# Kernel tuning notes

Hardware: AMD Instinct MI355X
Metric: run time of the kernel (lower is better)

The kernel has to match this reference:

```python
import jax, jax.numpy as jnp
import numpy as np

B, S, D, H, F = 2, 2048, 1024, 16, 4096
DH = D // H
EPS = 1e-6


def setup_inputs() -> dict:
    key = jax.random.key(0)
    ks = jax.random.split(key, 8)
    x = jax.random.normal(ks[0], (B, S, D), dtype=jnp.float32)
    # causal mask, broadcastable over [B,H,S,S]
    attention_mask = jnp.tril(jnp.ones((S, S), dtype=bool))[None, None]
    Wqkv = jax.random.normal(ks[1], (3 * D, D), dtype=jnp.float32) * (1.0 / np.sqrt(D))
    Wout = jax.random.normal(ks[2], (D, D), dtype=jnp.float32) * (1.0 / np.sqrt(D))
    W1 = jax.random.normal(ks[3], (F, D), dtype=jnp.float32) * (1.0 / np.sqrt(D))
    b1 = jnp.zeros((F,), dtype=jnp.float32)
    W2 = jax.random.normal(ks[4], (D, F), dtype=jnp.float32) * (1.0 / np.sqrt(F))
    b2 = jnp.zeros((D,), dtype=jnp.float32)
    gamma1 = jnp.ones((D,), dtype=jnp.float32)
    beta1 = jnp.zeros((D,), dtype=jnp.float32)
    gamma2 = jnp.ones((D,), dtype=jnp.float32)
    beta2 = jnp.zeros((D,), dtype=jnp.float32)
    return {"x": x, "attention_mask": attention_mask, "Wqkv": Wqkv, "Wout": Wout,
            "W1": W1, "b1": b1, "W2": W2, "b2": b2,
            "gamma1": gamma1, "beta1": beta1, "gamma2": gamma2, "beta2": beta2}


def layer_norm(x, gamma, beta):
    # Matches torch module: (x - mean) / (std + eps), std unbiased=False
    mean = jnp.mean(x, axis=-1, keepdims=True)
    std = jnp.sqrt(jnp.mean((x - mean) ** 2, axis=-1, keepdims=True))
    return gamma * ((x - mean) / (std + EPS)) + beta


def reference(x, attention_mask, Wqkv, Wout, W1, b1, W2, b2, gamma1, beta1, gamma2, beta2):
    # --- attention sub-block (Pre-LN) ---
    h = layer_norm(x, gamma1, beta1)
    qkv = h @ Wqkv.T                                   # [B,S,3D]
    qkv = qkv.reshape(B, S, 3, H, DH).transpose(2, 0, 3, 1, 4)  # [3,B,H,S,DH]
    q, k, v = qkv[0], qkv[1], qkv[2]
    scale = DH ** -0.5
    scores = jnp.einsum('bhqd,bhkd->bhqk', q, k) * scale
    scores = jnp.where(attention_mask, scores, -jnp.inf)
    attn = jax.nn.softmax(scores, axis=-1)
    out = jnp.einsum('bhqk,bhkd->bhqd', attn, v)       # [B,H,S,DH]
    out = out.transpose(0, 2, 1, 3).reshape(B, S, D)
    out = out @ Wout.T
    x = x + out                                        # dropout eval = identity
    # --- FFN sub-block (Pre-LN) ---
    h = layer_norm(x, gamma2, beta2)
    h = jax.nn.gelu(h @ W1.T + b1, approximate=False)  # torch GELU default = exact erf
    h = h @ W2.T + b2
    return x + h
```

## Files before the change

### kernel.cpp

```cpp
#include <hip/hip_runtime.h>
#include <hip/hip_bf16.h>
#include <math.h>


typedef __bf16 bf16;
typedef __bf16 bf16x4 __attribute__((ext_vector_type(4)));
typedef __bf16 bf16x8 __attribute__((ext_vector_type(8)));
typedef float f32x4 __attribute__((ext_vector_type(4)));

#define LOG2E 1.4426950408889634f
#define NSHIFT -17.312340489f

__device__ __forceinline__ f32x4 mfma16(bf16x8 a, bf16x8 b, f32x4 c) {
    return __builtin_amdgcn_mfma_f32_16x16x32_bf16(a, b, c, 0, 0, 0);
}
__device__ __forceinline__ void load16_lds(const bf16* g, bf16* l) {
    __builtin_amdgcn_global_load_lds(
        (__attribute__((address_space(1))) void*)g,
        (__attribute__((address_space(3))) void*)l, 16, 0, 0);
}

__global__ __launch_bounds__(256) void cvt4_kernel(const float* __restrict__ s0,
                                                   const float* __restrict__ s1,
                                                   const float* __restrict__ s2,
                                                   const float* __restrict__ s3,
                                                   bf16* __restrict__ dst) {
    const int blk = blockIdx.x;
    const float* s;
    int base;
    if (blk < 3072)      { s = s0; base = blk * 1024; }
    else if (blk < 4096) { s = s1; base = (blk - 3072) * 1024; }
    else if (blk < 8192) { s = s2; base = (blk - 4096) * 1024; }
    else                 { s = s3; base = (blk - 8192) * 1024; }
    const int t4 = threadIdx.x * 4;
    const float4 f = *(const float4*)(s + base + t4);
    bf16x4 o;
    o[0] = (bf16)f.x; o[1] = (bf16)f.y; o[2] = (bf16)f.z; o[3] = (bf16)f.w;
    *(bf16x4*)(dst + (size_t)blk * 1024 + t4) = o;
}

__global__ __launch_bounds__(256) void ln_kernel(const float* __restrict__ xin,
                                                 bf16* __restrict__ out,
                                                 const float* __restrict__ gamma,
                                                 const float* __restrict__ beta) {
    const int row = blockIdx.x;
    const int tid = threadIdx.x;
    const float4 f = *(const float4*)(xin + (size_t)row * 1024 + tid * 4);
    float v[4] = {f.x, f.y, f.z, f.w};
    float s = v[0] + v[1] + v[2] + v[3];
    float s2 = v[0] * v[0] + v[1] * v[1] + v[2] * v[2] + v[3] * v[3];
#pragma unroll
    for (int off = 1; off < 64; off <<= 1) {
        s += __shfl_xor(s, off);
        s2 += __shfl_xor(s2, off);
    }
    __shared__ float red[8];
    const int wave = tid >> 6, lane = tid & 63;
    if (lane == 0) { red[wave] = s; red[4 + wave] = s2; }
    __syncthreads();
    s = red[0] + red[1] + red[2] + red[3];
    s2 = red[4] + red[5] + red[6] + red[7];
    const float mean = s * (1.0f / 1024.0f);
    float var = s2 * (1.0f / 1024.0f) - mean * mean;
    var = fmaxf(var, 0.0f);
    const float rstd = 1.0f / (sqrtf(var) + 1e-6f);
    const int c = tid * 4;
    const float4 g = *(const float4*)(gamma + c);
    const float4 b = *(const float4*)(beta + c);
    bf16x4 o;
    o[0] = (bf16)((v[0] - mean) * rstd * g.x + b.x);
    o[1] = (bf16)((v[1] - mean) * rstd * g.y + b.y);
    o[2] = (bf16)((v[2] - mean) * rstd * g.z + b.z);
    o[3] = (bf16)((v[3] - mean) * rstd * g.w + b.w);
    *(bf16x4*)(out + (size_t)row * 1024 + c) = o;
}

#define STAGE(tt, bi)                                              \
    do {                                                           \
        const int _k0 = (tt) << 5;                                 \
        load16_lds(Ap + _k0, &As[bi][tid * 8]);                    \
        load16_lds(Bp + _k0, &Bs[bi][tid * 8]);                    \
        load16_lds(Ap + rstep + _k0, &As[bi][tid * 8 + 2048]);     \
        load16_lds(Bp + rstep + _k0, &Bs[bi][tid * 8 + 2048]);     \
    } while (0)

__global__ __launch_bounds__(256, 3) void gemm_res(const bf16* __restrict__ A,
                                                   const bf16* __restrict__ B,
                                                   int N, int K, int ldk,
                                                   float* __restrict__ outf,
                                                   const float* __restrict__ resf) {
    __shared__ alignas(16) bf16 As[3][128 * 32];
    __shared__ alignas(16) bf16 Bs[3][128 * 32];
    const int tid = threadIdx.x;
    const int bm = blockIdx.x, bn = blockIdx.y;
    const int wave = tid >> 6, lane = tid & 63;
    const int wm = (wave >> 1) * 64, wn = (wave & 1) * 64;
    const int l16 = lane & 15, quad = lane >> 4;

    f32x4 acc[4][4] = {};

    const int row0 = tid >> 2, ch0 = tid & 3;
    const int gch = ch0 ^ ((row0 >> 1) & 3);
    const bf16* Ap = A + (size_t)(bm * 128 + row0) * ldk + gch * 8;
    const bf16* Bp = B + (size_t)(bn * 128 + row0) * ldk + gch * 8;
    const size_t rstep = (size_t)64 * ldk;

    const int nt = K >> 5;

    STAGE(0, 0);
    STAGE(1, 1);
    asm volatile("s_waitcnt vmcnt(4)" ::: "memory");
    __builtin_amdgcn_s_barrier();
    asm volatile("" ::: "memory");

    int i0 = 0, i1 = 1, i2 = 2;
    for (int t = 0; t < nt; ++t) {
        if (t + 2 < nt) STAGE(t + 2, i2);

        bf16x8 af[4], bfr[4];
#pragma unroll
        for (int i = 0; i < 4; i++) {
            const int ra = wm + i * 16 + l16;
            af[i] = *(const bf16x8*)(&As[i0][ra * 32 + (quad ^ ((ra >> 1) & 3)) * 8]);
        }
#pragma unroll
        for (int j = 0; j < 4; j++) {
            const int rb = wn + j * 16 + l16;
            bfr[j] = *(const bf16x8*)(&Bs[i0][rb * 32 + (quad ^ ((rb >> 1) & 3)) * 8]);
        }
        __builtin_amdgcn_s_setprio(1);
#pragma unroll
        for (int i = 0; i < 4; i++)
#pragma unroll
            for (int j = 0; j < 4; j++) acc[i][j] = mfma16(af[i], bfr[j], acc[i][j]);
        __builtin_amdgcn_s_setprio(0);

        if (t + 2 < nt) {
            asm volatile("s_waitcnt vmcnt(4)" ::: "memory");
        } else if (t + 1 < nt) {
            asm volatile("s_waitcnt vmcnt(0)" ::: "memory");
        }
        if (t + 1 < nt) {
            __builtin_amdgcn_s_barrier();
            asm volatile("" ::: "memory");
        }
        const int tmp = i0; i0 = i1; i1 = i2; i2 = tmp;
    }

#pragma unroll
    for (int i = 0; i < 4; i++)
#pragma unroll
        for (int j = 0; j < 4; j++) {
            const int gr0 = bm * 128 + wm + i * 16 + quad * 4;
            const int gc = bn * 128 + wn + j * 16 + l16;
#pragma unroll
            for (int r = 0; r < 4; r++) {
                const size_t idx = (size_t)(gr0 + r) * N + gc;
                outf[idx] = acc[i][j][r] + resf[idx];
            }
        }
}
#undef STAGE

#define STG_A(bb, rk, tt)                                          \
    do {                                                           \
        const int _ko = ((tt) << 6) + ((rk) << 5);                 \
        load16_lds(Ap + _ko, &As[bb][rk][tid * 8]);                \
        load16_lds(Ap + rstep + _ko, &As[bb][rk][4096 + tid * 8]); \
    } while (0)
#define STG_B(bb, rk, tt)                                          \
    do {                                                           \
        const int _ko = ((tt) << 6) + ((rk) << 5);                 \
        load16_lds(Bp + _ko, &Bs[bb][rk][tid * 8]);                \
        load16_lds(Bp + rstep + _ko, &Bs[bb][rk][4096 + tid * 8]); \
    } while (0)
#define PHASE_OPEN()                       \
    __builtin_amdgcn_s_barrier();          \
    asm volatile("" ::: "memory");         \
    __builtin_amdgcn_s_setprio(1)
#define PHASE_CLOSE()                      \
    __builtin_amdgcn_s_setprio(0);         \
    __builtin_amdgcn_s_barrier();          \
    asm volatile("" ::: "memory")

template <int EPI>
__global__ __launch_bounds__(512, 2) void gemm256_8ph(const bf16* __restrict__ A,
                                                      const bf16* __restrict__ B,
                                                      int N, int K, int ldk,
                                                      bf16* __restrict__ outb,
                                                      float* __restrict__ outf,
                                                      const float* __restrict__ bias,
                                                      bf16* __restrict__ qk,
                                                      bf16* __restrict__ vt) {
    __shared__ alignas(16) bf16 As[2][2][8192];
    __shared__ alignas(16) bf16 Bs[2][2][8192];
    const int tid = threadIdx.x;
    const int bm = blockIdx.x, bn = blockIdx.y;
    const int wave = tid >> 6, lane = tid & 63;
    const int wm = (wave >> 2) * 128, wn = (wave & 3) * 64;
    const int l16 = lane & 15, quad = lane >> 4;

    f32x4 acc[8][4] = {};

    const size_t koff = (size_t)blockIdx.z * K;
    const int row0 = tid >> 2;
    const int gch = (tid & 3) ^ (row0 & 3);
    const bf16* Ap = A + (size_t)(bm * 256 + row0) * ldk + koff + gch * 8;
    const bf16* Bp = B + (size_t)(bn * 256 + row0) * ldk + koff + gch * 8;
    const size_t rstep = (size_t)128 * ldk;

    const int NT = K >> 6;

    STG_A(0, 0, 0); STG_B(0, 0, 0); STG_A(0, 1, 0); STG_B(0, 1, 0);
    STG_A(1, 0, 1); STG_B(1, 0, 1); STG_A(1, 1, 1);
    asm volatile("s_waitcnt vmcnt(6)" ::: "memory");
    __builtin_amdgcn_s_barrier();
    asm volatile("" ::: "memory");

    for (int t = 0; t < NT; ++t) {
        const int buf = t & 1;
        bf16x8 af[8], bj0, bj1;

#pragma unroll
        for (int i = 0; i < 8; i++) {
            const int ra = wm + i * 16 + l16;
            af[i] = *(const bf16x8*)&As[buf][0][ra * 32 + (quad ^ (ra & 3)) * 8];
        }
        {
            const int rb0 = wn + l16, rb1 = wn + 16 + l16;
            bj0 = *(const bf16x8*)&Bs[buf][0][rb0 * 32 + (quad ^ (rb0 & 3)) * 8];
            bj1 = *(const bf16x8*)&Bs[buf][0][rb1 * 32 + (quad ^ (rb1 & 3)) * 8];
        }
        if (t + 1 < NT) STG_B(buf ^ 1, 1, t + 1);
        PHASE_OPEN();
#pragma unroll
        for (int i = 0; i < 8; i++) {
            acc[i][0] = mfma16(af[i], bj0, acc[i][0]);
            acc[i][1] = mfma16(af[i], bj1, acc[i][1]);
        }
        PHASE_CLOSE();

        {
            const int rb2 = wn + 32 + l16, rb3 = wn + 48 + l16;
            bj0 = *(const bf16x8*)&Bs[buf][0][rb2 * 32 + (quad ^ (rb2 & 3)) * 8];
            bj1 = *(const bf16x8*)&Bs[buf][0][rb3 * 32 + (quad ^ (rb3 & 3)) * 8];
        }
        if (t + 2 < NT) STG_A(buf, 0, t + 2);
        PHASE_OPEN();
#pragma unroll
        for (int i = 0; i < 8; i++) {
            acc[i][2] = mfma16(af[i], bj0, acc[i][2]);
            acc[i][3] = mfma16(af[i], bj1, acc[i][3]);
        }
        PHASE_CLOSE();

#pragma unroll
        for (int i = 0; i < 8; i++) {
            const int ra = wm + i * 16 + l16;
            af[i] = *(const bf16x8*)&As[buf][1][ra * 32 + (quad ^ (ra & 3)) * 8];
        }
        {
            const int rb0 = wn + l16, rb1 = wn + 16 + l16;
            bj0 = *(const bf16x8*)&Bs[buf][1][rb0 * 32 + (quad ^ (rb0 & 3)) * 8];
            bj1 = *(const bf16x8*)&Bs[buf][1][rb1 * 32 + (quad ^ (rb1 & 3)) * 8];
        }
        if (t + 2 < NT) STG_B(buf, 0, t + 2);
        PHASE_OPEN();
#pragma unroll
        for (int i = 0; i < 8; i++) {
            acc[i][0] = mfma16(af[i], bj0, acc[i][0]);
            acc[i][1] = mfma16(af[i], bj1, acc[i][1]);
        }
        PHASE_CLOSE();

        {
            const int rb2 = wn + 32 + l16, rb3 = wn + 48 + l16;
            bj0 = *(const bf16x8*)&Bs[buf][1][rb2 * 32 + (quad ^ (rb2 & 3)) * 8];
            bj1 = *(const bf16x8*)&Bs[buf][1][rb3 * 32 + (quad ^ (rb3 & 3)) * 8];
        }
        if (t + 2 < NT) STG_A(buf, 1, t + 2);
        __builtin_amdgcn_s_barrier();
        asm volatile("" ::: "memory");
        __builtin_amdgcn_s_setprio(1);
#pragma unroll
        for (int i = 0; i < 8; i++) {
            acc[i][2] = mfma16(af[i], bj0, acc[i][2]);
            acc[i][3] = mfma16(af[i], bj1, acc[i][3]);
        }
        __builtin_amdgcn_s_setprio(0);
        if (t + 2 < NT) {
            asm volatile("s_waitcnt vmcnt(6)" ::: "memory");
        } else if (t + 1 < NT) {
            asm volatile("s_waitcnt vmcnt(0)" ::: "memory");
        }
        if (t + 1 < NT) {
            __builtin_amdgcn_s_barrier();
            asm volatile("" ::: "memory");
        }
    }

#pragma unroll
    for (int i = 0; i < 8; i++) {
#pragma unroll
        for (int j = 0; j < 4; j++) {
            const int gr0 = bm * 256 + wm + i * 16 + quad * 4;
            const int gc = bn * 256 + wn + j * 16 + l16;
            float bv = 0.0f;
            if (EPI == 2) bv = bias[gc];
            if (EPI == 5 && bias && blockIdx.z == 0) bv = bias[gc];
            if (EPI == 4 && gc >= 2048) {
                const int n = gc - 2048;
                const int hh = n >> 6, dd = n & 63;
                const int bb = gr0 >> 11, ss = gr0 & 2047;
                bf16x4 pk;
#pragma unroll
                for (int r = 0; r < 4; r++) pk[r] = (bf16)acc[i][j][r];
                *(bf16x4*)(vt + ((size_t)((bb * 16 + hh) * 64 + dd)) * 2048 + ss) = pk;
            } else {
#pragma unroll
                for (int r = 0; r < 4; r++) {
                    const float v = acc[i][j][r];
                    const size_t idx = (size_t)(gr0 + r) * N + gc;
                    if (EPI == 2) {
                        const float t = v + bv;
                        outb[idx] = (bf16)(0.5f * t * (1.0f + erff(t * 0.70710678118654752f)));
                    } else if (EPI == 5) {
                        atomicAdd(&outf[idx], v + bv);
                    } else {
                        qk[(size_t)(gr0 + r) * 2048 + gc] = (bf16)v;
                    }
                }
            }
        }
    }
}
#undef STG_A
#undef STG_B
#undef PHASE_OPEN
#undef PHASE_CLOSE

__global__ __launch_bounds__(256, 4) void flash_attn(const bf16* __restrict__ qk,
                                                     const bf16* __restrict__ vt,
                                                     bf16* __restrict__ attn) {
    __shared__ alignas(16) bf16 Ks[64 * 72];
    __shared__ alignas(16) bf16 Vs[64 * 72];
    __shared__ alignas(16) bf16 Ps[4][16 * 72];
    const int tid = threadIdx.x;
    const int wave = tid >> 6, lane = tid & 63;
    const int l16 = lane & 15, quad = lane >> 4;
    const int bh = blockIdx.x;
    const int qt = 31 - blockIdx.y;
    const int b = bh >> 4, h = bh & 15;
    const int q0w = qt * 64 + wave * 16;
    const bf16* qkb = qk + (size_t)b * 2048 * 2048;
    const bf16* vtb = vt + (size_t)bh * 64 * 2048;

    bf16x8 qf[2];
#pragma unroll
    for (int c = 0; c < 2; c++) {
        bf16x8 v = *(const bf16x8*)(qkb + (size_t)(q0w + l16) * 2048 +
                                    h * 64 + c * 32 + quad * 8);
#pragma unroll
        for (int e = 0; e < 8; e++) v[e] = (bf16)((float)v[e] * 0.125f);
        qf[c] = v;
    }

    float lsum[4] = {0.0f, 0.0f, 0.0f, 0.0f};
    f32x4 o[4] = {};

    const int ntiles = qt + 1;
    for (int t = 0; t < ntiles; t++) {
        const int k0 = t * 64;
#pragma unroll
        for (int i = 0; i < 2; i++) {
            const int r = i * 32 + (tid >> 3), ch = tid & 7;
            *(uint4*)(&Ks[r * 72 + ch * 8]) =
                *(const uint4*)(qkb + (size_t)(k0 + r) * 2048 + 1024 + h * 64 + ch * 8);
            *(uint4*)(&Vs[r * 72 + ch * 8]) =
                *(const uint4*)(vtb + (size_t)r * 2048 + k0 + ch * 8);
        }
        __syncthreads();
        f32x4 s[4];
#pragma unroll
        for (int kt = 0; kt < 4; kt++) {
            const bf16x8 k0f = *(const bf16x8*)(&Ks[(kt * 16 + l16) * 72 + quad * 8]);
            const bf16x8 k1f = *(const bf16x8*)(&Ks[(kt * 16 + l16) * 72 + 32 + quad * 8]);
            s[kt] = mfma16(qf[1], k1f, mfma16(qf[0], k0f, (f32x4){0, 0, 0, 0}));
        }
        const bool need_mask = (t == ntiles - 1);
#pragma unroll
        for (int r = 0; r < 4; r++) {
            const int qrow = q0w + quad * 4 + r;
            float e0 = exp2f(fmaf(s[0][r], LOG2E, NSHIFT));
            float e1 = exp2f(fmaf(s[1][r], LOG2E, NSHIFT));
            float e2 = exp2f(fmaf(s[2][r], LOG2E, NSHIFT));
            float e3 = exp2f(fmaf(s[3][r], LOG2E, NSHIFT));
            if (need_mask) {
                if (k0 + l16 > qrow) e0 = 0.0f;
                if (k0 + 16 + l16 > qrow) e1 = 0.0f;
                if (k0 + 32 + l16 > qrow) e2 = 0.0f;
                if (k0 + 48 + l16 > qrow) e3 = 0.0f;
            }
            lsum[r] += (e0 + e1) + (e2 + e3);
            bf16* pp = &Ps[wave][(quad * 4 + r) * 72];
            pp[l16] = (bf16)e0;
            pp[16 + l16] = (bf16)e1;
            pp[32 + l16] = (bf16)e2;
            pp[48 + l16] = (bf16)e3;
        }
#pragma unroll
        for (int c = 0; c < 2; c++) {
            const bf16x8 pf = *(const bf16x8*)(&Ps[wave][l16 * 72 + c * 32 + quad * 8]);
#pragma unroll
            for (int dt = 0; dt < 4; dt++) {
                const bf16x8 vf =
                    *(const bf16x8*)(&Vs[(dt * 16 + l16) * 72 + c * 32 + quad * 8]);
                o[dt] = mfma16(pf, vf, o[dt]);
            }
        }
        __syncthreads();
    }

#pragma unroll
    for (int r = 0; r < 4; r++) {
#pragma unroll
        for (int off = 1; off < 16; off <<= 1) lsum[r] += __shfl_xor(lsum[r], off);
        lsum[r] = 1.0f / fmaxf(lsum[r], 1e-30f);
    }
    bf16* ob = attn + (size_t)b * 2048 * 1024;
#pragma unroll
    for (int dt = 0; dt < 4; dt++)
#pragma unroll
        for (int r = 0; r < 4; r++) {
            const int q = q0w + quad * 4 + r;
            ob[(size_t)q * 1024 + h * 64 + dt * 16 + l16] = (bf16)(o[dt][r] * lsum[r]);
        }
}

extern "C" void kernel_launch(void* const* d_in, const int* in_sizes, int n_in,
                              void* d_out, int out_size, void* d_ws, size_t ws_size,
                              hipStream_t stream) {
    const float* x    = (const float*)d_in[0];
    const float* Wqkv = (const float*)d_in[2];
    const float* Wout = (const float*)d_in[3];
    const float* W1   = (const float*)d_in[4];
    const float* b1   = (const float*)d_in[5];
    const float* W2   = (const float*)d_in[6];
    const float* b2   = (const float*)d_in[7];
    const float* g1   = (const float*)d_in[8];
    const float* be1  = (const float*)d_in[9];
    const float* g2   = (const float*)d_in[10];
    const float* be2  = (const float*)d_in[11];

    char* ws = (char*)d_ws;
    bf16* Wb     = (bf16*)(ws);
    bf16* Wqkv_b = (bf16*)(ws);
    bf16* Wout_b = (bf16*)(ws + (6u << 20));
    bf16* W1_b   = (bf16*)(ws + (8u << 20));
    bf16* W2_b   = (bf16*)(ws + (16u << 20));
    bf16* h      = (bf16*)(ws + (24u << 20));
    bf16* qkbuf  = (bf16*)(ws + (32u << 20));
    bf16* vtbuf  = (bf16*)(ws + (48u << 20));
    bf16* attn   = (bf16*)(ws + (56u << 20));
    bf16* act    = (bf16*)(ws + (32u << 20));
    float* x2    = (float*)d_out;

    cvt4_kernel<<<12288, 256, 0, stream>>>(Wqkv, Wout, W1, W2, Wb);

    ln_kernel<<<4096, 256, 0, stream>>>(x, h, g1, be1);
    gemm256_8ph<4><<<dim3(16, 12), 512, 0, stream>>>(h, Wqkv_b, 3072, 1024, 1024,
                                                     nullptr, nullptr, nullptr,
                                                     qkbuf, vtbuf);
    flash_attn<<<dim3(32, 32), 256, 0, stream>>>(qkbuf, vtbuf, attn);
    gemm_res<<<dim3(32, 8), 256, 0, stream>>>(attn, Wout_b, 1024, 1024, 1024, x2, x);
    ln_kernel<<<4096, 256, 0, stream>>>(x2, h, g2, be2);
    gemm256_8ph<2><<<dim3(16, 16), 512, 0, stream>>>(h, W1_b, 4096, 1024, 1024,
                                                     act, nullptr, b1, nullptr, nullptr);
    gemm256_8ph<5><<<dim3(16, 4, 4), 512, 0, stream>>>(act, W2_b, 1024, 1024, 4096,
                                                       nullptr, x2, b2, nullptr, nullptr);
}
```

Measured before the change: 407.8 us.

## Simplify output-projection GEMM to double buffering, change LDS swizzle, add attention setprio

Replaces the output-projection GEMM's triple-buffered pipeline, which used explicit vmcnt waits, with a simpler double-buffered loop that issues a __syncthreads each iteration. The kernel becomes templated on its epilogue. The 256-tile GEMM's LDS swizzle changes from (row & 3) to ((row >> 1) & 3) to alter the bank-conflict pattern. The flash attention kernel raises wave priority around its MFMA sections. The simpler GEMM pipeline trades away prefetch depth and may expose more load latency.

```diff
diff --git a/kernel.cpp b/kernel.cpp
--- a/kernel.cpp
+++ b/kernel.cpp
@@ -75,22 +75,16 @@
     *(bf16x4*)(out + (size_t)row * 1024 + c) = o;
 }
 
-#define STAGE(tt, bi)                                              \
-    do {                                                           \
-        const int _k0 = (tt) << 5;                                 \
-        load16_lds(Ap + _k0, &As[bi][tid * 8]);                    \
-        load16_lds(Bp + _k0, &Bs[bi][tid * 8]);                    \
-        load16_lds(Ap + rstep + _k0, &As[bi][tid * 8 + 2048]);     \
-        load16_lds(Bp + rstep + _k0, &Bs[bi][tid * 8 + 2048]);     \
-    } while (0)
-
-__global__ __launch_bounds__(256, 3) void gemm_res(const bf16* __restrict__ A,
-                                                   const bf16* __restrict__ B,
-                                                   int N, int K, int ldk,
-                                                   float* __restrict__ outf,
-                                                   const float* __restrict__ resf) {
-    __shared__ alignas(16) bf16 As[3][128 * 32];
-    __shared__ alignas(16) bf16 Bs[3][128 * 32];
+template <int EPI>
+__global__ __launch_bounds__(256, 3) void gemm_bt(const bf16* __restrict__ A,
+                                                  const bf16* __restrict__ B,
+                                                  int N, int K, int ldk,
+                                                  bf16* __restrict__ outb,
+                                                  float* __restrict__ outf,
+                                                  const float* __restrict__ bias,
+                                                  const float* __restrict__ resf) {
+    __shared__ alignas(16) bf16 As[2][128 * 32];
+    __shared__ alignas(16) bf16 Bs[2][128 * 32];
     const int tid = threadIdx.x;
     const int bm = blockIdx.x, bn = blockIdx.y;
     const int wave = tid >> 6, lane = tid & 63;
@@ -105,62 +99,59 @@
     const bf16* Bp = B + (size_t)(bn * 128 + row0) * ldk + gch * 8;
     const size_t rstep = (size_t)64 * ldk;
 
-    const int nt = K >> 5;
-
-    STAGE(0, 0);
-    STAGE(1, 1);
-    asm volatile("s_waitcnt vmcnt(4)" ::: "memory");
-    __builtin_amdgcn_s_barrier();
-    asm volatile("" ::: "memory");
-
-    int i0 = 0, i1 = 1, i2 = 2;
-    for (int t = 0; t < nt; ++t) {
-        if (t + 2 < nt) STAGE(t + 2, i2);
-
+#pragma unroll
+    for (int r = 0; r < 2; r++) {
+        load16_lds(Ap + r * rstep, &As[0][tid * 8 + r * 2048]);
+        load16_lds(Bp + r * rstep, &Bs[0][tid * 8 + r * 2048]);
+    }
+    __syncthreads();
+
+    int buf = 0;
+    for (int k0 = 0; k0 < K; k0 += 32, buf ^= 1) {
+        if (k0 + 32 < K) {
+#pragma unroll
+            for (int r = 0; r < 2; r++) {
+                load16_lds(Ap + r * rstep + k0 + 32, &As[buf ^ 1][tid * 8 + r * 2048]);
+                load16_lds(Bp + r * rstep + k0 + 32, &Bs[buf ^ 1][tid * 8 + r * 2048]);
+            }
+        }
         bf16x8 af[4], bfr[4];
 #pragma unroll
         for (int i = 0; i < 4; i++) {
             const int ra = wm + i * 16 + l16;
-            af[i] = *(const bf16x8*)(&As[i0][ra * 32 + (quad ^ ((ra >> 1) & 3)) * 8]);
+            af[i] = *(const bf16x8*)(&As[buf][ra * 32 + (quad ^ ((ra >> 1) & 3)) * 8]);
         }
 #pragma unroll
         for (int j = 0; j < 4; j++) {
             const int rb = wn + j * 16 + l16;
-            bfr[j] = *(const bf16x8*)(&Bs[i0][rb * 32 + (quad ^ ((rb >> 1) & 3)) * 8]);
-        }
-        __builtin_amdgcn_s_setprio(1);
+            bfr[j] = *(const bf16x8*)(&Bs[buf][rb * 32 + (quad ^ ((rb >> 1) & 3)) * 8]);
+        }
 #pragma unroll
         for (int i = 0; i < 4; i++)
 #pragma unroll
             for (int j = 0; j < 4; j++) acc[i][j] = mfma16(af[i], bfr[j], acc[i][j]);
-        __builtin_amdgcn_s_setprio(0);
-
-        if (t + 2 < nt) {
-            asm volatile("s_waitcnt vmcnt(4)" ::: "memory");
-        } else if (t + 1 < nt) {
-            asm volatile("s_waitcnt vmcnt(0)" ::: "memory");
-        }
-        if (t + 1 < nt) {
-            __builtin_amdgcn_s_barrier();
-            asm volatile("" ::: "memory");
-        }
-        const int tmp = i0; i0 = i1; i1 = i2; i2 = tmp;
-    }
-
-#pragma unroll
-    for (int i = 0; i < 4; i++)
+        __syncthreads();
+    }
+
+#pragma unroll
+    for (int i = 0; i < 4; i++) {
 #pragma unroll
         for (int j = 0; j < 4; j++) {
             const int gr0 = bm * 128 + wm + i * 16 + quad * 4;
             const int gc = bn * 128 + wn + j * 16 + l16;
 #pragma unroll
             for (int r = 0; r < 4; r++) {
+                const float v = acc[i][j][r];
                 const size_t idx = (size_t)(gr0 + r) * N + gc;
-                outf[idx] = acc[i][j][r] + resf[idx];
+                if (EPI == 1) {
+                    outf[idx] = v + resf[idx];
+                } else {
+                    outb[idx] = (bf16)v;
+                }
             }
         }
-}
-#undef STAGE
+    }
+}
 
 #define STG_A(bb, rk, tt)                                          \
     do {                                                           \
@@ -204,7 +195,7 @@
 
     const size_t koff = (size_t)blockIdx.z * K;
     const int row0 = tid >> 2;
-    const int gch = (tid & 3) ^ (row0 & 3);
+    const int gch = (tid & 3) ^ ((row0 >> 1) & 3);
     const bf16* Ap = A + (size_t)(bm * 256 + row0) * ldk + koff + gch * 8;
     const bf16* Bp = B + (size_t)(bn * 256 + row0) * ldk + koff + gch * 8;
     const size_t rstep = (size_t)128 * ldk;
@@ -224,12 +215,12 @@
 #pragma unroll
         for (int i = 0; i < 8; i++) {
             const int ra = wm + i * 16 + l16;
-            af[i] = *(const bf16x8*)&As[buf][0][ra * 32 + (quad ^ (ra & 3)) * 8];
+            af[i] = *(const bf16x8*)&As[buf][0][ra * 32 + (quad ^ ((ra >> 1) & 3)) * 8];
         }
         {
             const int rb0 = wn + l16, rb1 = wn + 16 + l16;
-            bj0 = *(const bf16x8*)&Bs[buf][0][rb0 * 32 + (quad ^ (rb0 & 3)) * 8];
-            bj1 = *(const bf16x8*)&Bs[buf][0][rb1 * 32 + (quad ^ (rb1 & 3)) * 8];
+            bj0 = *(const bf16x8*)&Bs[buf][0][rb0 * 32 + (quad ^ ((rb0 >> 1) & 3)) * 8];
+            bj1 = *(const bf16x8*)&Bs[buf][0][rb1 * 32 + (quad ^ ((rb1 >> 1) & 3)) * 8];
         }
         if (t + 1 < NT) STG_B(buf ^ 1, 1, t + 1);
         PHASE_OPEN();
@@ -242,8 +233,8 @@
 
         {
             const int rb2 = wn + 32 + l16, rb3 = wn + 48 + l16;
-            bj0 = *(const bf16x8*)&Bs[buf][0][rb2 * 32 + (quad ^ (rb2 & 3)) * 8];
-            bj1 = *(const bf16x8*)&Bs[buf][0][rb3 * 32 + (quad ^ (rb3 & 3)) * 8];
+            bj0 = *(const bf16x8*)&Bs[buf][0][rb2 * 32 + (quad ^ ((rb2 >> 1) & 3)) * 8];
+            bj1 = *(const bf16x8*)&Bs[buf][0][rb3 * 32 + (quad ^ ((rb3 >> 1) & 3)) * 8];
         }
         if (t + 2 < NT) STG_A(buf, 0, t + 2);
         PHASE_OPEN();
@@ -257,12 +248,12 @@
 #pragma unroll
         for (int i = 0; i < 8; i++) {
             const int ra = wm + i * 16 + l16;
-            af[i] = *(const bf16x8*)&As[buf][1][ra * 32 + (quad ^ (ra & 3)) * 8];
+            af[i] = *(const bf16x8*)&As[buf][1][ra * 32 + (quad ^ ((ra >> 1) & 3)) * 8];
         }
         {
             const int rb0 = wn + l16, rb1 = wn + 16 + l16;
-            bj0 = *(const bf16x8*)&Bs[buf][1][rb0 * 32 + (quad ^ (rb0 & 3)) * 8];
-            bj1 = *(const bf16x8*)&Bs[buf][1][rb1 * 32 + (quad ^ (rb1 & 3)) * 8];
+            bj0 = *(const bf16x8*)&Bs[buf][1][rb0 * 32 + (quad ^ ((rb0 >> 1) & 3)) * 8];
+            bj1 = *(const bf16x8*)&Bs[buf][1][rb1 * 32 + (quad ^ ((rb1 >> 1) & 3)) * 8];
         }
         if (t + 2 < NT) STG_B(buf, 0, t + 2);
         PHASE_OPEN();
@@ -275,8 +266,8 @@
 
         {
             const int rb2 = wn + 32 + l16, rb3 = wn + 48 + l16;
-            bj0 = *(const bf16x8*)&Bs[buf][1][rb2 * 32 + (quad ^ (rb2 & 3)) * 8];
-            bj1 = *(const bf16x8*)&Bs[buf][1][rb3 * 32 + (quad ^ (rb3 & 3)) * 8];
+            bj0 = *(const bf16x8*)&Bs[buf][1][rb2 * 32 + (quad ^ ((rb2 >> 1) & 3)) * 8];
+            bj1 = *(const bf16x8*)&Bs[buf][1][rb3 * 32 + (quad ^ ((rb3 >> 1) & 3)) * 8];
         }
         if (t + 2 < NT) STG_A(buf, 1, t + 2);
         __builtin_amdgcn_s_barrier();
@@ -381,12 +372,14 @@
         }
         __syncthreads();
         f32x4 s[4];
+        __builtin_amdgcn_s_setprio(1);
 #pragma unroll
         for (int kt = 0; kt < 4; kt++) {
             const bf16x8 k0f = *(const bf16x8*)(&Ks[(kt * 16 + l16) * 72 + quad * 8]);
             const bf16x8 k1f = *(const bf16x8*)(&Ks[(kt * 16 + l16) * 72 + 32 + quad * 8]);
             s[kt] = mfma16(qf[1], k1f, mfma16(qf[0], k0f, (f32x4){0, 0, 0, 0}));
         }
+        __builtin_amdgcn_s_setprio(0);
         const bool need_mask = (t == ntiles - 1);
 #pragma unroll
         for (int r = 0; r < 4; r++) {
@@ -408,6 +401,7 @@
             pp[32 + l16] = (bf16)e2;
             pp[48 + l16] = (bf16)e3;
         }
+        __builtin_amdgcn_s_setprio(1);
 #pragma unroll
         for (int c = 0; c < 2; c++) {
             const bf16x8 pf = *(const bf16x8*)(&Ps[wave][l16 * 72 + c * 32 + quad * 8]);
@@ -418,6 +412,7 @@
                 o[dt] = mfma16(pf, vf, o[dt]);
             }
         }
+        __builtin_amdgcn_s_setprio(0);
         __syncthreads();
     }
 
@@ -472,7 +467,8 @@
                                                      nullptr, nullptr, nullptr,
                                                      qkbuf, vtbuf);
     flash_attn<<<dim3(32, 32), 256, 0, stream>>>(qkbuf, vtbuf, attn);
-    gemm_res<<<dim3(32, 8), 256, 0, stream>>>(attn, Wout_b, 1024, 1024, 1024, x2, x);
+    gemm_bt<1><<<dim3(32, 8), 256, 0, stream>>>(attn, Wout_b, 1024, 1024, 1024,
+                                                nullptr, x2, nullptr, x);
     ln_kernel<<<4096, 256, 0, stream>>>(x2, h, g2, be2);
     gemm256_8ph<2><<<dim3(16, 16), 512, 0, stream>>>(h, W1_b, 4096, 1024, 1024,
                                                      act, nullptr, b1, nullptr, nullptr);
```

Result: faster. 385.2 us (-5.5%).
